# Optimization experiments

Hardware: AMD Instinct MI355X
Metric: run time of the kernel (lower is better)

The kernel has to match this reference:

```python
import jax, jax.numpy as jnp
import numpy as np

N_NODES = 100000
N_EDGES = 3200000
IN_FEATS = 256
N_HIDDEN = 256
N_CLASSES = 40


def setup_inputs() -> dict:
    key = jax.random.key(0)
    ks = jax.random.split(key, 8)
    features = jax.random.normal(ks[0], (N_NODES, IN_FEATS), dtype=jnp.float32)
    src = jax.random.randint(ks[1], (N_EDGES,), 0, N_NODES, dtype=jnp.int64)
    dst = jax.random.randint(ks[2], (N_EDGES,), 0, N_NODES, dtype=jnp.int64)
    # Glorot-ish init scaled down for stability
    W0 = jax.random.normal(ks[3], (IN_FEATS, N_HIDDEN), dtype=jnp.float32) * (1.0 / np.sqrt(IN_FEATS))
    W1 = jax.random.normal(ks[4], (N_HIDDEN, N_HIDDEN), dtype=jnp.float32) * (1.0 / np.sqrt(N_HIDDEN))
    W2 = jax.random.normal(ks[5], (N_HIDDEN, N_CLASSES), dtype=jnp.float32) * (1.0 / np.sqrt(N_HIDDEN))
    b0 = jnp.zeros((N_HIDDEN,), jnp.float32)
    b1 = jnp.zeros((N_HIDDEN,), jnp.float32)
    b2 = jnp.zeros((N_CLASSES,), jnp.float32)
    return {"features": features, "src": src, "dst": dst,
            "W0": W0, "b0": b0, "W1": W1, "b1": b1, "W2": W2, "b2": b2}


def _degree_norms(src, dst, n_nodes):
    ones = jnp.ones(src.shape[0], jnp.float32)
    deg_out = jax.ops.segment_sum(ones, src, num_segments=n_nodes)
    deg_in = jax.ops.segment_sum(ones, dst, num_segments=n_nodes)
    # DGL norm='both': clamp degree to >=1 before rsqrt
    norm_out = jax.lax.rsqrt(jnp.maximum(deg_out, 1.0))  # applied on source side
    norm_in = jax.lax.rsqrt(jnp.maximum(deg_in, 1.0))    # applied on dest side
    return norm_out, norm_in


def _graph_conv(h, src, dst, norm_out, norm_in, W, b, activation):
    # h: [N, Fin]. norm='both': D_in^{-1/2} * A * (D_out^{-1/2} * h) @ W + b
    in_f, out_f = W.shape
    h = h * norm_out[:, None]
    if in_f > out_f:
        # mult weight first to reduce message width (DGL optimization, same math)
        h = h @ W
        agg = jax.ops.segment_sum(h[src], dst, num_segments=h.shape[0])
    else:
        agg = jax.ops.segment_sum(h[src], dst, num_segments=h.shape[0])
        agg = agg @ W
    out = agg * norm_in[:, None] + b
    if activation is not None:
        out = activation(out)
    return out


def reference(features, src, dst, W0, b0, W1, b1, W2, b2):
    n = features.shape[0]
    norm_out, norm_in = _degree_norms(src, dst, n)
    h = _graph_conv(features, src, dst, norm_out, norm_in, W0, b0, jax.nn.relu)
    h = _graph_conv(h, src, dst, norm_out, norm_in, W1, b1, jax.nn.relu)
    h = _graph_conv(h, src, dst, norm_out, norm_in, W2, b2, None)
    return h
```

## Files before the change

kernel.cpp:

```cpp
#include <hip/hip_runtime.h>

#define NN 100000
#define NE 3200000
#define F 256
#define NCLS 40
#define NC 391
#define NBLK_H 256
#define EPB (NE / NBLK_H)
#define CW 25000

using h4 = __attribute__((ext_vector_type(4))) _Float16;
using h8 = __attribute__((ext_vector_type(8))) _Float16;
using f4 = __attribute__((ext_vector_type(4))) float;

__global__ __launch_bounds__(512) void hist_k(const int* __restrict__ src,
                                              const int* __restrict__ dst,
                                              unsigned* __restrict__ pcnt,
                                              unsigned* __restrict__ pcc) {
    __shared__ unsigned hsrc[CW];
    __shared__ unsigned hc[NC];
    int t = threadIdx.x, b = blockIdx.x;
    for (int i = t; i < CW; i += 512) hsrc[i] = 0;
    for (int i = t; i < NC; i += 512) hc[i] = 0;
    __syncthreads();
    int beg = b * EPB, end = beg + EPB;
    for (int e = beg + t; e < end; e += 512) {
        int s = src[e];
        atomicAdd(&hsrc[s >> 2], 1u << (8 * (s & 3)));
        atomicAdd(&hc[dst[e] >> 8], 1u);
    }
    __syncthreads();
    unsigned* pc = pcnt + (size_t)b * CW;
    for (int i = t; i < CW; i += 512) pc[i] = hsrc[i];
    unsigned* pb = pcc + (size_t)b * NC;
    for (int i = t; i < NC; i += 512) pb[i] = hc[i];
}

__global__ __launch_bounds__(256) void redA_k(const unsigned* __restrict__ pcnt,
                                              unsigned* __restrict__ cntlo,
                                              unsigned* __restrict__ cnthi) {
    int w = blockIdx.x * 256 + threadIdx.x;
    if (w >= CW) return;
    int g = blockIdx.y;
    unsigned lo = 0, hi = 0;
    for (int b = g * 32; b < g * 32 + 32; b++) {
        unsigned v = pcnt[(size_t)b * CW + w];
        lo += (v & 255u) | (((v >> 8) & 255u) << 16);
        hi += ((v >> 16) & 255u) | ((v >> 24) << 16);
    }
    atomicAdd(&cntlo[w], lo);
    atomicAdd(&cnthi[w], hi);
}

__global__ void nout2_k(const unsigned* __restrict__ cntlo,
                        const unsigned* __restrict__ cnthi,
                        float* __restrict__ nout) {
    int w = blockIdx.x * blockDim.x + threadIdx.x;
    if (w >= CW) return;
    unsigned lo = cntlo[w], hi = cnthi[w];
    float4 o;
    o.x = rsqrtf(fmaxf((float)(lo & 0xFFFFu), 1.f));
    o.y = rsqrtf(fmaxf((float)(lo >> 16), 1.f));
    o.z = rsqrtf(fmaxf((float)(hi & 0xFFFFu), 1.f));
    o.w = rsqrtf(fmaxf((float)(hi >> 16), 1.f));
    *(float4*)(nout + w * 4) = o;
}

__global__ __launch_bounds__(256) void offsets_k(const unsigned* __restrict__ pcc,
                                                 unsigned* __restrict__ curoff,
                                                 unsigned* __restrict__ totals) {
    __shared__ unsigned sh[256];
    int c = blockIdx.x, t = threadIdx.x;
    unsigned v = pcc[(size_t)t * NC + c];
    sh[t] = v;
    __syncthreads();
    for (int off = 1; off < 256; off <<= 1) {
        unsigned x = (t >= off) ? sh[t - off] : 0;
        __syncthreads();
        sh[t] += x;
        __syncthreads();
    }
    curoff[(size_t)t * NC + c] = sh[t] - v;
    if (t == 255) totals[c] = sh[255];
}

__global__ __launch_bounds__(512) void base_k(const unsigned* __restrict__ totals,
                                              int* __restrict__ cbase) {
    __shared__ unsigned sh[512];
    int t = threadIdx.x;
    unsigned v = (t < NC) ? totals[t] : 0;
    sh[t] = v;
    __syncthreads();
    for (int off = 1; off < 512; off <<= 1) {
        unsigned x = (t >= off) ? sh[t - off] : 0;
        __syncthreads();
        sh[t] += x;
        __syncthreads();
    }
    if (t < NC) cbase[t] = (int)(sh[t] - v);
    if (t == 0) cbase[NC] = NE;
}

__global__ __launch_bounds__(512) void p1scat_k(const int* __restrict__ src,
                                                const int* __restrict__ dst,
                                                const int* __restrict__ cbase,
                                                const unsigned* __restrict__ curoff,
                                                unsigned* __restrict__ ebuf) {
    __shared__ int cur[NC];
    int t = threadIdx.x, b = blockIdx.x;
    for (int i = t; i < NC; i += 512)
        cur[i] = cbase[i] + (int)curoff[(size_t)b * NC + i];
    __syncthreads();
    int beg = b * EPB, end = beg + EPB;
    for (int e = beg + t; e < end; e += 512) {
        int d = dst[e];
        int p = atomicAdd(&cur[d >> 8], 1);
        ebuf[p] = (unsigned)src[e] | ((unsigned)(d & 255) << 17);
    }
}

__global__ __launch_bounds__(512) void p2build_k(const int* __restrict__ cbase,
                                                 const unsigned* __restrict__ ebuf,
                                                 int* __restrict__ csr_src,
                                                 int* __restrict__ row_ptr,
                                                 float* __restrict__ nin) {
    __shared__ int cnt[256], cur[256], sh[256];
    int c = blockIdx.x, t = threadIdx.x;
    int beg = cbase[c], end = cbase[c + 1];
    if (t < 256) cnt[t] = 0;
    __syncthreads();
    for (int e = beg + t; e < end; e += 512)
        atomicAdd(&cnt[(ebuf[e] >> 17) & 255], 1);
    __syncthreads();
    int v = 0;
    if (t < 256) { v = cnt[t]; sh[t] = v; }
    __syncthreads();
    for (int off = 1; off < 256; off <<= 1) {
        int x = (t < 256 && t >= off) ? sh[t - off] : 0;
        __syncthreads();
        if (t < 256) sh[t] += x;
        __syncthreads();
    }
    if (t < 256) {
        int pref = sh[t] - v;
        int node = c * 256 + t;
        if (node <= NN) row_ptr[node] = beg + pref;
        if (node < NN)  nin[node] = rsqrtf(fmaxf((float)v, 1.f));
        cur[t] = pref;
    }
    if (c == 0 && t == 0) row_ptr[NN] = NE;
    __syncthreads();
    for (int e = beg + t; e < end; e += 512) {
        unsigned w = ebuf[e];
        int p = atomicAdd(&cur[(w >> 17) & 255], 1);
        csr_src[beg + p] = (int)(w & 0x1FFFFu);
    }
}

__global__ void conv_fused_k(const float4* __restrict__ fin, const float* __restrict__ nout,
                             h4* __restrict__ fout,
                             const float* __restrict__ W0, const float* __restrict__ W1,
                             const float* __restrict__ W2,
                             _Float16* __restrict__ Wt0, _Float16* __restrict__ Wt1,
                             _Float16* __restrict__ Wt2) {
    int i = blockIdx.x * blockDim.x + threadIdx.x;
    const int N4 = NN * 64;
    if (i < N4) {
        float s = nout[i >> 6];
        float4 v = fin[i];
        h4 o;
        o[0] = (_Float16)(v.x * s);
        o[1] = (_Float16)(v.y * s);
        o[2] = (_Float16)(v.z * s);
        o[3] = (_Float16)(v.w * s);
        fout[i] = o;
    } else {
        int j = i - N4;
        if (j < 65536) {
            int n = j >> 8, k = j & 255;
            Wt0[j] = (_Float16)W0[k * 256 + n];
        } else if (j < 131072) {
            int jj = j - 65536;
            int n = jj >> 8, k = jj & 255;
            Wt1[jj] = (_Float16)W1[k * 256 + n];
        } else if (j < 147456) {
            int jj = j - 131072;
            int n = jj >> 8, k = jj & 255;
            Wt2[jj] = (n < NCLS) ? (_Float16)W2[k * NCLS + n] : (_Float16)0.0f;
        }
    }
}

__global__ __launch_bounds__(256) void agg256h_k(
        const int* __restrict__ row_ptr, const int* __restrict__ csr_src,
        const _Float16* __restrict__ h, _Float16* __restrict__ agg, int nN) {
    int node = (blockIdx.x * blockDim.x + threadIdx.x) >> 6;
    int lane = threadIdx.x & 63;
    if (node >= nN) return;
    int half = lane >> 5, col = lane & 31;
    int beg = row_ptr[node], end = row_ptr[node + 1];
    f4 a[4][2];
#pragma unroll
    for (int u = 0; u < 4; u++) { a[u][0] = (f4){0,0,0,0}; a[u][1] = (f4){0,0,0,0}; }
    int e = beg;
    for (; e + 7 < end; e += 8) {
        int s[4];
#pragma unroll
        for (int u = 0; u < 4; u++) s[u] = csr_src[e + 2 * u + half];
        h8 v[4];
#pragma unroll
        for (int u = 0; u < 4; u++)
            v[u] = *(const h8*)(h + (size_t)s[u] * F + col * 8);
#pragma unroll
        for (int u = 0; u < 4; u++)
#pragma unroll
            for (int j = 0; j < 8; j++) a[u][j >> 2][j & 3] += (float)v[u][j];
    }
    for (int t = e + half; t < end; t += 2) {
        h8 v = *(const h8*)(h + (size_t)csr_src[t] * F + col * 8);
#pragma unroll
        for (int j = 0; j < 8; j++) a[0][j >> 2][j & 3] += (float)v[j];
    }
    float r[8];
#pragma unroll
    for (int j = 0; j < 8; j++)
        r[j] = (a[0][j >> 2][j & 3] + a[1][j >> 2][j & 3])
             + (a[2][j >> 2][j & 3] + a[3][j >> 2][j & 3]);
#pragma unroll
    for (int j = 0; j < 8; j++) r[j] += __shfl_xor(r[j], 32);
    if (half == 0) {
        h8 o;
#pragma unroll
        for (int j = 0; j < 8; j++) o[j] = (_Float16)r[j];
        *(h8*)(agg + (size_t)node * F + col * 8) = o;
    }
}

__global__ __launch_bounds__(256) void agg64h_k(
        const int* __restrict__ row_ptr, const int* __restrict__ csr_src,
        const _Float16* __restrict__ t3, const float* __restrict__ nin,
        const float* __restrict__ b2, float* __restrict__ out, int nN) {
    int node = (blockIdx.x * blockDim.x + threadIdx.x) >> 6;
    int lane = threadIdx.x & 63;
    if (node >= nN) return;
    int grp = lane >> 3, c = lane & 7;
    int beg = row_ptr[node], end = row_ptr[node + 1];
    float a0[8], a1[8];
#pragma unroll
    for (int j = 0; j < 8; j++) { a0[j] = 0.f; a1[j] = 0.f; }
    int e = beg;
    for (; e + 15 < end; e += 16) {
        int s0 = csr_src[e + grp], s1 = csr_src[e + 8 + grp];
        h8 v0 = *(const h8*)(t3 + (size_t)s0 * 64 + c * 8);
        h8 v1 = *(const h8*)(t3 + (size_t)s1 * 64 + c * 8);
#pragma unroll
        for (int j = 0; j < 8; j++) { a0[j] += (float)v0[j]; a1[j] += (float)v1[j]; }
    }
    for (int t = e + grp; t < end; t += 8) {
        h8 v = *(const h8*)(t3 + (size_t)csr_src[t] * 64 + c * 8);
#pragma unroll
        for (int j = 0; j < 8; j++) a0[j] += (float)v[j];
    }
    float r[8];
#pragma unroll
    for (int j = 0; j < 8; j++) {
        r[j] = a0[j] + a1[j];
        r[j] += __shfl_xor(r[j], 8);
        r[j] += __shfl_xor(r[j], 16);
        r[j] += __shfl_xor(r[j], 32);
    }
    if (grp == 0 && c < 5) {
        float ni = nin[node];
        float4 o;
        o.x = r[0] * ni + b2[c * 8 + 0];
        o.y = r[1] * ni + b2[c * 8 + 1];
        o.z = r[2] * ni + b2[c * 8 + 2];
        o.w = r[3] * ni + b2[c * 8 + 3];
        *(float4*)(out + (size_t)node * NCLS + c * 8) = o;
        o.x = r[4] * ni + b2[c * 8 + 4];
        o.y = r[5] * ni + b2[c * 8 + 5];
        o.z = r[6] * ni + b2[c * 8 + 6];
        o.w = r[7] * ni + b2[c * 8 + 7];
        *(float4*)(out + (size_t)node * NCLS + c * 8 + 4) = o;
    }
}

template <int NT, int EPI>
__global__ __launch_bounds__(1024) void gemm_lds_k(
        const _Float16* __restrict__ A, const _Float16* __restrict__ Wt,
        _Float16* __restrict__ C, int M,
        const float* __restrict__ nin, const float* __restrict__ nout,
        const float* __restrict__ bias) {
    constexpr int COLS = NT * 16;
    __shared__ _Float16 lds[COLS * 256];
    char* ldsb = (char*)lds;

    const int tid  = threadIdx.x;
    const int lane = tid & 63;
    const int w    = tid >> 6;
    const int row0 = blockIdx.x * 256;

#pragma unroll
    for (int i = 0; i < COLS / 32; i++) {
        int idx  = (i * 1024 + tid) * 8;
        int byte = idx * 2;
        int row  = byte >> 9;
        int swz  = byte ^ ((row & 7) << 4);
        *(h8*)(ldsb + swz) = *(const h8*)(Wt + idx);
    }

    int arow = row0 + w * 16 + (lane & 15);
    if (arow >= M) arow = M - 1;
    const _Float16* Ap = A + (size_t)arow * 256 + (lane >> 4) * 8;
    h8 areg[8];
#pragma unroll
    for (int i = 0; i < 8; i++) areg[i] = *(const h8*)(Ap + i * 32);

    __syncthreads();

    f4 acc[NT];
#pragma unroll
    for (int n = 0; n < NT; n++) acc[n] = (f4){0.f, 0.f, 0.f, 0.f};

#pragma unroll
    for (int k0 = 0; k0 < 8; k0++) {
        int kb = (k0 * 32 + (lane >> 4) * 8) * 2;
#pragma unroll
        for (int n = 0; n < NT; n++) {
            int r    = n * 16 + (lane & 15);
            int byte = r * 512 + kb;
            int swz  = byte ^ ((r & 7) << 4);
            h8 bf = *(const h8*)(ldsb + swz);
            acc[n] = __builtin_amdgcn_mfma_f32_16x16x32_f16(areg[k0], bf, acc[n], 0, 0, 0);
        }
    }

    __syncthreads();

    const int g  = lane >> 4;
    const int rb = row0 + w * 16 + g * 4;
    float si[4], so[4];
    if (EPI) {
#pragma unroll
        for (int r = 0; r < 4; r++) {
            int rr = rb + r; if (rr >= M) rr = M - 1;
            si[r] = nin[rr];
            so[r] = nout[rr];
        }
    }
    char* warea = ldsb + w * (16 * COLS * 2);
#pragma unroll
    for (int n = 0; n < NT; n++) {
        float bb = EPI ? bias[n * 16 + (lane & 15)] : 0.f;
#pragma unroll
        for (int r = 0; r < 4; r++) {
            float x = acc[n][r];
            if (EPI) x = fmaxf(x * si[r] + bb, 0.f) * so[r];
            int lrow = g * 4 + r;
            int lcol = n * 16 + (lane & 15);
            *(_Float16*)(warea + (size_t)(lrow * COLS + lcol) * 2) = (_Float16)x;
        }
    }

    _Float16* Crow = C + (size_t)(row0 + w * 16) * COLS;
#pragma unroll
    for (int i = 0; i < COLS / 32; i++) {
        int off  = i * 1024 + lane * 16;
        int lrow = off / (COLS * 2);
        int grow = row0 + w * 16 + lrow;
        h8 v = *(const h8*)(warea + off);
        if (grow < M) *(h8*)((char*)Crow + off) = v;
    }
}

extern "C" void kernel_launch(void* const* d_in, const int* in_sizes, int n_in,
                              void* d_out, int out_size, void* d_ws, size_t ws_size,
                              hipStream_t stream) {
    const float* features = (const float*)d_in[0];
    const int*   src      = (const int*)d_in[1];
    const int*   dst      = (const int*)d_in[2];
    const float* W0       = (const float*)d_in[3];
    const float* b0       = (const float*)d_in[4];
    const float* W1       = (const float*)d_in[5];
    const float* b1       = (const float*)d_in[6];
    const float* W2       = (const float*)d_in[7];
    const float* b2       = (const float*)d_in[8];
    float* out = (float*)d_out;

    char* ws = (char*)d_ws;
    const size_t H_BYTES = (size_t)NN * F * 2;
    _Float16* hA   = (_Float16*)(ws);
    _Float16* hB   = (_Float16*)(ws + H_BYTES);
    _Float16* t3h  = (_Float16*)(ws + 2 * H_BYTES);
    char* q = ws + 2 * H_BYTES + (size_t)NN * 64 * 2;
    int* csr_src    = (int*)q;               q += (size_t)NE * 4;
    unsigned* ebuf  = (unsigned*)q;          q += (size_t)NE * 4;
    unsigned* pcnt  = (unsigned*)q;          q += (size_t)NBLK_H * CW * 4;
    unsigned* pcc   = (unsigned*)q;          q += (size_t)NBLK_H * NC * 4 + 1024;
    unsigned* curoff= (unsigned*)q;          q += (size_t)NBLK_H * NC * 4 + 1024;
    char* p = q;
    const size_t SB = 401408;
    unsigned* totals = (unsigned*)(p + 0 * SB);
    int*   cbase   = (int*)(p + 1 * SB);
    int*   row_ptr = (int*)(p + 2 * SB);
    float* nout    = (float*)(p + 3 * SB);
    float* nin     = (float*)(p + 4 * SB);
    unsigned* cntlo = (unsigned*)(p + 5 * SB);
    unsigned* cnthi = (unsigned*)(p + 6 * SB);
    _Float16* Wt0  = (_Float16*)(p + 7 * SB);
    _Float16* Wt1  = (_Float16*)(p + 7 * SB + 131072);
    _Float16* Wt2  = (_Float16*)(p + 7 * SB + 262144);

    const int AGG_BLOCKS = (NN * 64 + 255) / 256;
    const int GB = (NN + 255) / 256;

    hipMemsetAsync(cntlo, 0, CW * 4, stream);
    hipMemsetAsync(cnthi, 0, CW * 4, stream);
    hist_k<<<NBLK_H, 512, 0, stream>>>(src, dst, pcnt, pcc);
    {
        dim3 rg((CW + 255) / 256, 8);
        redA_k<<<rg, 256, 0, stream>>>(pcnt, cntlo, cnthi);
    }
    nout2_k<<<(CW + 255) / 256, 256, 0, stream>>>(cntlo, cnthi, nout);
    offsets_k<<<NC, 256, 0, stream>>>(pcc, curoff, totals);
    base_k<<<1, 512, 0, stream>>>(totals, cbase);
    p1scat_k<<<NBLK_H, 512, 0, stream>>>(src, dst, cbase, curoff, ebuf);
    p2build_k<<<NC, 512, 0, stream>>>(cbase, ebuf, csr_src, row_ptr, nin);

    {
        int total = NN * 64 + 147456;
        conv_fused_k<<<(total + 255) / 256, 256, 0, stream>>>(
            (const float4*)features, nout, (h4*)hB, W0, W1, W2, Wt0, Wt1, Wt2);
    }

    agg256h_k<<<AGG_BLOCKS, 256, 0, stream>>>(row_ptr, csr_src, hB, hA, NN);
    gemm_lds_k<16, 1><<<GB, 1024, 0, stream>>>(hA, Wt0, hB, NN, nin, nout, b0);

    agg256h_k<<<AGG_BLOCKS, 256, 0, stream>>>(row_ptr, csr_src, hB, hA, NN);
    gemm_lds_k<16, 1><<<GB, 1024, 0, stream>>>(hA, Wt1, hB, NN, nin, nout, b1);

    gemm_lds_k<4, 0><<<GB, 1024, 0, stream>>>(hB, Wt2, t3h, NN, nullptr, nullptr, nullptr);
    agg64h_k<<<AGG_BLOCKS, 256, 0, stream>>>(row_ptr, csr_src, t3h, nin, b2, out, NN);
}
```

Measured before the change: 840.7 us.

## Fuse layer-1 and layer-2 GEMMs, pre-swizzle weights, drop atomic degree reduction

Merges the second 256x256 GEMM and the 256x40 GEMM into one kernel. The activated layer-1 tile stays in LDS and is fed straight into the second MFMA pass, so the 100000x256 fp16 intermediate is never written to or reread from global memory. The weight transpose now applies the XOR swizzle at pack time, so the LDS fill is a plain copy. The degree reduction writes per-group partials and sums them in nout2_k, which removes the two memsets and the atomics. The fused kernel adds extra LDS traffic and barriers per block.

Measured after the change: 837.0 us. No clear change (-0.4%).

```diff
diff --git a/kernel.cpp b/kernel.cpp
--- a/kernel.cpp
+++ b/kernel.cpp
@@ -37,8 +37,8 @@
 }
 
 __global__ __launch_bounds__(256) void redA_k(const unsigned* __restrict__ pcnt,
-                                              unsigned* __restrict__ cntlo,
-                                              unsigned* __restrict__ cnthi) {
+                                              unsigned* __restrict__ pl,
+                                              unsigned* __restrict__ ph) {
     int w = blockIdx.x * 256 + threadIdx.x;
     if (w >= CW) return;
     int g = blockIdx.y;
@@ -48,16 +48,17 @@
         lo += (v & 255u) | (((v >> 8) & 255u) << 16);
         hi += ((v >> 16) & 255u) | ((v >> 24) << 16);
     }
-    atomicAdd(&cntlo[w], lo);
-    atomicAdd(&cnthi[w], hi);
-}
-
-__global__ void nout2_k(const unsigned* __restrict__ cntlo,
-                        const unsigned* __restrict__ cnthi,
+    pl[(size_t)g * CW + w] = lo;
+    ph[(size_t)g * CW + w] = hi;
+}
+
+__global__ void nout2_k(const unsigned* __restrict__ pl, const unsigned* __restrict__ ph,
                         float* __restrict__ nout) {
     int w = blockIdx.x * blockDim.x + threadIdx.x;
     if (w >= CW) return;
-    unsigned lo = cntlo[w], hi = cnthi[w];
+    unsigned lo = 0, hi = 0;
+#pragma unroll
+    for (int g = 0; g < 8; g++) { lo += pl[(size_t)g * CW + w]; hi += ph[(size_t)g * CW + w]; }
     float4 o;
     o.x = rsqrtf(fmaxf((float)(lo & 0xFFFFu), 1.f));
     o.y = rsqrtf(fmaxf((float)(lo >> 16), 1.f));
@@ -177,15 +178,15 @@
     } else {
         int j = i - N4;
         if (j < 65536) {
-            int n = j >> 8, k = j & 255;
+            int n = j >> 8, k = (j & 255) ^ ((n & 7) << 3);
             Wt0[j] = (_Float16)W0[k * 256 + n];
         } else if (j < 131072) {
             int jj = j - 65536;
-            int n = jj >> 8, k = jj & 255;
+            int n = jj >> 8, k = (jj & 255) ^ ((n & 7) << 3);
             Wt1[jj] = (_Float16)W1[k * 256 + n];
         } else if (j < 147456) {
             int jj = j - 131072;
-            int n = jj >> 8, k = jj & 255;
+            int n = jj >> 8, k = (jj & 255) ^ ((n & 7) << 3);
             Wt2[jj] = (n < NCLS) ? (_Float16)W2[k * NCLS + n] : (_Float16)0.0f;
         }
     }
@@ -285,28 +286,22 @@
     }
 }
 
-template <int NT, int EPI>
-__global__ __launch_bounds__(1024) void gemm_lds_k(
+__global__ __launch_bounds__(1024) void gemm0_k(
         const _Float16* __restrict__ A, const _Float16* __restrict__ Wt,
         _Float16* __restrict__ C, int M,
         const float* __restrict__ nin, const float* __restrict__ nout,
         const float* __restrict__ bias) {
-    constexpr int COLS = NT * 16;
-    __shared__ _Float16 lds[COLS * 256];
+    __shared__ _Float16 lds[256 * 256];
     char* ldsb = (char*)lds;
-
     const int tid  = threadIdx.x;
     const int lane = tid & 63;
     const int w    = tid >> 6;
     const int row0 = blockIdx.x * 256;
 
 #pragma unroll
-    for (int i = 0; i < COLS / 32; i++) {
-        int idx  = (i * 1024 + tid) * 8;
-        int byte = idx * 2;
-        int row  = byte >> 9;
-        int swz  = byte ^ ((row & 7) << 4);
-        *(h8*)(ldsb + swz) = *(const h8*)(Wt + idx);
+    for (int i = 0; i < 8; i++) {
+        int idx = (i * 1024 + tid) * 8;
+        *(h8*)(ldsb + idx * 2) = *(const h8*)(Wt + idx);
     }
 
     int arow = row0 + w * 16 + (lane & 15);
@@ -318,19 +313,18 @@
 
     __syncthreads();
 
-    f4 acc[NT];
-#pragma unroll
-    for (int n = 0; n < NT; n++) acc[n] = (f4){0.f, 0.f, 0.f, 0.f};
+    f4 acc[16];
+#pragma unroll
+    for (int n = 0; n < 16; n++) acc[n] = (f4){0.f, 0.f, 0.f, 0.f};
 
 #pragma unroll
     for (int k0 = 0; k0 < 8; k0++) {
         int kb = (k0 * 32 + (lane >> 4) * 8) * 2;
 #pragma unroll
-        for (int n = 0; n < NT; n++) {
+        for (int n = 0; n < 16; n++) {
             int r    = n * 16 + (lane & 15);
             int byte = r * 512 + kb;
-            int swz  = byte ^ ((r & 7) << 4);
-            h8 bf = *(const h8*)(ldsb + swz);
+            h8 bf = *(const h8*)(ldsb + (byte ^ ((r & 7) << 4)));
             acc[n] = __builtin_amdgcn_mfma_f32_16x16x32_f16(areg[k0], bf, acc[n], 0, 0, 0);
         }
     }
@@ -340,36 +334,152 @@
     const int g  = lane >> 4;
     const int rb = row0 + w * 16 + g * 4;
     float si[4], so[4];
-    if (EPI) {
+#pragma unroll
+    for (int r = 0; r < 4; r++) {
+        int rr = rb + r; if (rr >= M) rr = M - 1;
+        si[r] = nin[rr];
+        so[r] = nout[rr];
+    }
+    char* warea = ldsb + w * 8192;
+#pragma unroll
+    for (int n = 0; n < 16; n++) {
+        float bb = bias[n * 16 + (lane & 15)];
 #pragma unroll
         for (int r = 0; r < 4; r++) {
-            int rr = rb + r; if (rr >= M) rr = M - 1;
-            si[r] = nin[rr];
-            so[r] = nout[rr];
-        }
-    }
-    char* warea = ldsb + w * (16 * COLS * 2);
-#pragma unroll
-    for (int n = 0; n < NT; n++) {
-        float bb = EPI ? bias[n * 16 + (lane & 15)] : 0.f;
-#pragma unroll
-        for (int r = 0; r < 4; r++) {
-            float x = acc[n][r];
-            if (EPI) x = fmaxf(x * si[r] + bb, 0.f) * so[r];
+            float x = fmaxf(acc[n][r] * si[r] + bb, 0.f) * so[r];
             int lrow = g * 4 + r;
             int lcol = n * 16 + (lane & 15);
-            *(_Float16*)(warea + (size_t)(lrow * COLS + lcol) * 2) = (_Float16)x;
-        }
-    }
-
-    _Float16* Crow = C + (size_t)(row0 + w * 16) * COLS;
-#pragma unroll
-    for (int i = 0; i < COLS / 32; i++) {
+            *(_Float16*)(warea + (size_t)(lrow * 256 + lcol) * 2) = (_Float16)x;
+        }
+    }
+
+    _Float16* Crow = C + (size_t)(row0 + w * 16) * 256;
+#pragma unroll
+    for (int i = 0; i < 8; i++) {
         int off  = i * 1024 + lane * 16;
-        int lrow = off / (COLS * 2);
+        int lrow = off >> 9;
         int grow = row0 + w * 16 + lrow;
         h8 v = *(const h8*)(warea + off);
         if (grow < M) *(h8*)((char*)Crow + off) = v;
+    }
+}
+
+__global__ __launch_bounds__(1024) void gemm12_k(
+        const _Float16* __restrict__ A, const _Float16* __restrict__ Wt1s,
+        const _Float16* __restrict__ Wt2s, _Float16* __restrict__ t3, int M,
+        const float* __restrict__ nin, const float* __restrict__ nout,
+        const float* __restrict__ bias) {
+    __shared__ _Float16 lds[256 * 256];
+    char* ldsb = (char*)lds;
+    const int tid  = threadIdx.x;
+    const int lane = tid & 63;
+    const int w    = tid >> 6;
+    const int row0 = blockIdx.x * 256;
+
+#pragma unroll
+    for (int i = 0; i < 8; i++) {
+        int idx = (i * 1024 + tid) * 8;
+        *(h8*)(ldsb + idx * 2) = *(const h8*)(Wt1s + idx);
+    }
+
+    int arow = row0 + w * 16 + (lane & 15);
+    if (arow >= M) arow = M - 1;
+    const _Float16* Ap = A + (size_t)arow * 256 + (lane >> 4) * 8;
+    h8 areg[8];
+#pragma unroll
+    for (int i = 0; i < 8; i++) areg[i] = *(const h8*)(Ap + i * 32);
+
+    __syncthreads();
+
+    f4 acc[16];
+#pragma unroll
+    for (int n = 0; n < 16; n++) acc[n] = (f4){0.f, 0.f, 0.f, 0.f};
+#pragma unroll
+    for (int k0 = 0; k0 < 8; k0++) {
+        int kb = (k0 * 32 + (lane >> 4) * 8) * 2;
+#pragma unroll
+        for (int n = 0; n < 16; n++) {
+            int r    = n * 16 + (lane & 15);
+            int byte = r * 512 + kb;
+            h8 bf = *(const h8*)(ldsb + (byte ^ ((r & 7) << 4)));
+            acc[n] = __builtin_amdgcn_mfma_f32_16x16x32_f16(areg[k0], bf, acc[n], 0, 0, 0);
+        }
+    }
+
+    __syncthreads();
+
+    const int g  = lane >> 4;
+    const int rb = row0 + w * 16 + g * 4;
+    float si[4], so[4];
+#pragma unroll
+    for (int r = 0; r < 4; r++) {
+        int rr = rb + r; if (rr >= M) rr = M - 1;
+        si[r] = nin[rr];
+        so[r] = nout[rr];
+    }
+    char* warea = ldsb + w * 8192;
+#pragma unroll
+    for (int n = 0; n < 16; n++) {
+        float bb = bias[n * 16 + (lane & 15)];
+#pragma unroll
+        for (int r = 0; r < 4; r++) {
+            float x = fmaxf(acc[n][r] * si[r] + bb, 0.f) * so[r];
+            int lrow = g * 4 + r;
+            int lcol = n * 16 + (lane & 15);
+            int byte = lrow * 512 + lcol * 2;
+            *(_Float16*)(warea + (byte ^ ((lrow & 7) << 4))) = (_Float16)x;
+        }
+    }
+
+    h8 areg2[8];
+    {
+        int lr = lane & 15;
+#pragma unroll
+        for (int k0 = 0; k0 < 8; k0++) {
+            int byte = lr * 512 + k0 * 64 + (lane >> 4) * 16;
+            areg2[k0] = *(const h8*)(warea + (byte ^ ((lr & 7) << 4)));
+        }
+    }
+    __syncthreads();
+
+#pragma unroll
+    for (int i = 0; i < 2; i++) {
+        int idx = (i * 1024 + tid) * 8;
+        *(h8*)(ldsb + idx * 2) = *(const h8*)(Wt2s + idx);
+    }
+    __syncthreads();
+
+    f4 acc2[4];
+#pragma unroll
+    for (int n = 0; n < 4; n++) acc2[n] = (f4){0.f, 0.f, 0.f, 0.f};
+#pragma unroll
+    for (int k0 = 0; k0 < 8; k0++) {
+        int kb = k0 * 64 + (lane >> 4) * 16;
+#pragma unroll
+        for (int n = 0; n < 4; n++) {
+            int r    = n * 16 + (lane & 15);
+            int byte = r * 512 + kb;
+            h8 bf = *(const h8*)(ldsb + (byte ^ ((r & 7) << 4)));
+            acc2[n] = __builtin_amdgcn_mfma_f32_16x16x32_f16(areg2[k0], bf, acc2[n], 0, 0, 0);
+        }
+    }
+
+    char* tarea = ldsb + 32768 + w * 2048;
+#pragma unroll
+    for (int n = 0; n < 4; n++)
+#pragma unroll
+        for (int r = 0; r < 4; r++) {
+            int lrow = g * 4 + r;
+            int c = n * 16 + (lane & 15);
+            *(_Float16*)(tarea + lrow * 128 + c * 2) = (_Float16)acc2[n][r];
+        }
+#pragma unroll
+    for (int i = 0; i < 2; i++) {
+        int off  = i * 1024 + lane * 16;
+        int lrow = off >> 7;
+        int grow = row0 + w * 16 + lrow;
+        h8 v = *(const h8*)(tarea + off);
+        if (grow < M) *(h8*)((char*)t3 + (size_t)grow * 128 + (off & 127)) = v;
     }
 }
 
@@ -396,6 +506,8 @@
     int* csr_src    = (int*)q;               q += (size_t)NE * 4;
     unsigned* ebuf  = (unsigned*)q;          q += (size_t)NE * 4;
     unsigned* pcnt  = (unsigned*)q;          q += (size_t)NBLK_H * CW * 4;
+    unsigned* pl    = (unsigned*)q;          q += (size_t)8 * CW * 4;
+    unsigned* ph    = (unsigned*)q;          q += (size_t)8 * CW * 4;
     unsigned* pcc   = (unsigned*)q;          q += (size_t)NBLK_H * NC * 4 + 1024;
     unsigned* curoff= (unsigned*)q;          q += (size_t)NBLK_H * NC * 4 + 1024;
     char* p = q;
@@ -405,23 +517,19 @@
     int*   row_ptr = (int*)(p + 2 * SB);
     float* nout    = (float*)(p + 3 * SB);
     float* nin     = (float*)(p + 4 * SB);
-    unsigned* cntlo = (unsigned*)(p + 5 * SB);
-    unsigned* cnthi = (unsigned*)(p + 6 * SB);
-    _Float16* Wt0  = (_Float16*)(p + 7 * SB);
-    _Float16* Wt1  = (_Float16*)(p + 7 * SB + 131072);
-    _Float16* Wt2  = (_Float16*)(p + 7 * SB + 262144);
+    _Float16* Wt0  = (_Float16*)(p + 5 * SB);
+    _Float16* Wt1  = (_Float16*)(p + 5 * SB + 131072);
+    _Float16* Wt2  = (_Float16*)(p + 5 * SB + 262144);
 
     const int AGG_BLOCKS = (NN * 64 + 255) / 256;
     const int GB = (NN + 255) / 256;
 
-    hipMemsetAsync(cntlo, 0, CW * 4, stream);
-    hipMemsetAsync(cnthi, 0, CW * 4, stream);
     hist_k<<<NBLK_H, 512, 0, stream>>>(src, dst, pcnt, pcc);
     {
         dim3 rg((CW + 255) / 256, 8);
-        redA_k<<<rg, 256, 0, stream>>>(pcnt, cntlo, cnthi);
-    }
-    nout2_k<<<(CW + 255) / 256, 256, 0, stream>>>(cntlo, cnthi, nout);
+        redA_k<<<rg, 256, 0, stream>>>(pcnt, pl, ph);
+    }
+    nout2_k<<<(CW + 255) / 256, 256, 0, stream>>>(pl, ph, nout);
     offsets_k<<<NC, 256, 0, stream>>>(pcc, curoff, totals);
     base_k<<<1, 512, 0, stream>>>(totals, cbase);
     p1scat_k<<<NBLK_H, 512, 0, stream>>>(src, dst, cbase, curoff, ebuf);
@@ -434,11 +542,10 @@
     }
 
     agg256h_k<<<AGG_BLOCKS, 256, 0, stream>>>(row_ptr, csr_src, hB, hA, NN);
-    gemm_lds_k<16, 1><<<GB, 1024, 0, stream>>>(hA, Wt0, hB, NN, nin, nout, b0);
+    gemm0_k<<<GB, 1024, 0, stream>>>(hA, Wt0, hB, NN, nin, nout, b0);
 
     agg256h_k<<<AGG_BLOCKS, 256, 0, stream>>>(row_ptr, csr_src, hB, hA, NN);
-    gemm_lds_k<16, 1><<<GB, 1024, 0, stream>>>(hA, Wt1, hB, NN, nin, nout, b1);
-
-    gemm_lds_k<4, 0><<<GB, 1024, 0, stream>>>(hB, Wt2, t3h, NN, nullptr, nullptr, nullptr);
+    gemm12_k<<<GB, 1024, 0, stream>>>(hA, Wt1, Wt2, t3h, NN, nin, nout, b1);
+
     agg64h_k<<<AGG_BLOCKS, 256, 0, stream>>>(row_ptr, csr_src, t3h, nin, b2, out, NN);
 }
```
